# Kernel tuning notes

Hardware: AMD Instinct MI355X
Metric: run time of the kernel (lower is better)

## Reference

```python
import jax, jax.numpy as jnp
import numpy as np

SCENE = (128, 128, 8)      # (X, Y, Z) voxel grid
VOXEL_SIZE = 0.4
DOWNSAMPLE_Z = 2
NUM_HEADS = 8
NUM_POINTS = 4
LN_EPS = 1e-5


def _pix2vox(depth, K, E, voxel_origin):
    # depth [1,H,W]; K [1,3,3]; E [1,4,4]; voxel_origin [1,3]
    B, H, W = depth.shape
    gx, gy = jnp.meshgrid(jnp.arange(W, dtype=depth.dtype), jnp.arange(H, dtype=depth.dtype))
    pix = jnp.stack([gx, gy])                              # [2,H,W] -> (u, v) after flip in torch
    d = depth[:, None]                                     # [B,1,H,W]
    p_x = jnp.concatenate([pix[None] * d, d], 1).reshape(B, 3, -1)
    p_c = jnp.linalg.inv(K) @ p_x                          # camera coords [B,3,HW]
    p_c = jnp.concatenate([p_c, jnp.ones_like(p_c[:, :1])], 1)
    p_w = jnp.linalg.inv(E) @ p_c                          # world coords [B,4,HW]
    p_v = (jnp.swapaxes(p_w[:, :3], 1, 2) - voxel_origin[:, None, :]) / VOXEL_SIZE - 0.5
    p_v = p_v.at[..., 2].set(p_v[..., 2] / DOWNSAMPLE_Z)
    return jnp.trunc(p_v).astype(jnp.int32)               # torch .long() truncates toward 0


def _voxel_mask(p_v):
    X, Y, Z = SCENE
    p = p_v[0]                                             # [HW,3] (batch asserted == 1)
    valid = ((p[:, 0] >= 0) & (p[:, 0] < X) & (p[:, 1] >= 0) & (p[:, 1] < Y)
             & (p[:, 2] >= 0) & (p[:, 2] < Z))
    flat = jnp.where(valid, (p[:, 0] * Y + p[:, 1]) * Z + p[:, 2], 0)
    return jnp.zeros(X * Y * Z, dtype=bool).at[flat].max(valid)


def _ms_deform_attn(q, feats, ref, Wv, bv, Woff, boff, Wattw, battw, Wout, bout):
    # q [N,C]; feats: list of [C,Hl,Wl]; ref [N,2] normalized (shared across levels)
    N, C = q.shape
    hd = C // NUM_HEADS
    shapes = [(f.shape[1], f.shape[2]) for f in feats]
    L = len(feats)
    flat = jnp.concatenate([f.reshape(C, -1).T for f in feats], 0)      # [Lsum, C]
    value = (flat @ Wv.T + bv).reshape(-1, NUM_HEADS, hd)               # [Lsum, h, hd]
    off = (q @ Woff.T + boff).reshape(N, NUM_HEADS, L, NUM_POINTS, 2)
    w = jax.nn.softmax((q @ Wattw.T + battw).reshape(N, NUM_HEADS, L * NUM_POINTS), -1)
    w = w.reshape(N, NUM_HEADS, L, NUM_POINTS)
    normalizer = jnp.array([[wl, hl] for (hl, wl) in shapes], dtype=q.dtype)  # (W,H) per level
    loc = ref[:, None, None, None, :] + off / normalizer[None, None, :, None, :]
    h_idx = jnp.arange(NUM_HEADS)[None, :, None]
    out = jnp.zeros((N, NUM_HEADS, hd), q.dtype)
    start = 0
    for lvl, (Hl, Wl) in enumerate(shapes):
        v = value[start:start + Hl * Wl]                   # [Hl*Wl, h, hd]
        start += Hl * Wl
        # grid_sample bilinear, align_corners=False, zero padding
        x = loc[:, :, lvl, :, 0] * Wl - 0.5                # [N,h,P]
        y = loc[:, :, lvl, :, 1] * Hl - 0.5
        x0 = jnp.floor(x); y0 = jnp.floor(y)
        lx = x - x0; ly = y - y0
        x0i = x0.astype(jnp.int32); y0i = y0.astype(jnp.int32)
        samp = jnp.zeros((N, NUM_HEADS, NUM_POINTS, hd), q.dtype)
        for dy, dx, wgt in ((0, 0, (1 - lx) * (1 - ly)), (0, 1, lx * (1 - ly)),
                            (1, 0, (1 - lx) * ly), (1, 1, lx * ly)):
            xi = x0i + dx; yi = y0i + dy
            ok = (xi >= 0) & (xi < Wl) & (yi >= 0) & (yi < Hl)
            idx = jnp.where(ok, yi * Wl + xi, 0)
            g = v[idx, h_idx]                              # [N,h,P,hd] per-head gather
            samp = samp + g * (wgt * ok)[..., None]
        out = out + jnp.einsum('nhp,nhpd->nhd', w[:, :, lvl], samp)
    return out.reshape(N, C) @ Wout.T + bout


def _forward(scene_embed, feat0, feat1, feat2, depth, K, E, voxel_origin, ref_pix,
             Wv, bv, Woff, boff, Wattw, battw, Wout, bout, ln_g, ln_b):
    X, Y, Z = SCENE
    mask = _voxel_mask(_pix2vox(depth, K, E, voxel_origin))             # [N] bool
    q = scene_embed[0]                                                  # [N,C]
    attn = _ms_deform_attn(q, [feat0[0], feat1[0], feat2[0]], ref_pix[0],
                           Wv, bv, Woff, boff, Wattw, battw, Wout, bout)
    h = q + attn                                                        # residual (MSDeformAttn identity)
    mu = jnp.mean(h, -1, keepdims=True)
    var = jnp.mean((h - mu) ** 2, -1, keepdims=True)
    h = (h - mu) / jnp.sqrt(var + LN_EPS) * ln_g + ln_b                 # post-norm
    out = jnp.where(mask[:, None], h, q)                                # index_fov_back_to_voxels
    return out.T.reshape(1, -1, X, Y, Z)                                # nlc -> nchw [1,C,X,Y,Z]


def setup_inputs() -> dict:
    key = jax.random.key(0)
    ks = jax.random.split(key, 12)
    X, Y, Z = SCENE
    N = X * Y * Z
    C = 128
    H, W = 192, 640
    s = 0.02
    scene_embed = jax.random.normal(ks[0], (1, N, C), jnp.float32)
    feat0 = jax.random.normal(ks[1], (1, C, 48, 160), jnp.float32)
    feat1 = jax.random.normal(ks[2], (1, C, 24, 80), jnp.float32)
    feat2 = jax.random.normal(ks[3], (1, C, 12, 40), jnp.float32)
    depth = jax.random.uniform(ks[4], (1, H, W), jnp.float32, 1.0, 40.0)
    K = jnp.array([[[552.55, 0.0, 320.0], [0.0, 552.55, 96.0], [0.0, 0.0, 1.0]]], jnp.float32)
    E = jnp.eye(4, dtype=jnp.float32)[None]
    voxel_origin = jnp.array([[-25.6, -3.2, 0.0]], jnp.float32)
    ref_pix = jax.random.uniform(ks[5], (1, N, 2), jnp.float32)
    return {
        'scene_embed': scene_embed, 'feat0': feat0, 'feat1': feat1, 'feat2': feat2,
        'depth': depth, 'K': K, 'E': E, 'voxel_origin': voxel_origin, 'ref_pix': ref_pix,
        'Wv': jax.random.normal(ks[6], (C, C), jnp.float32) * s,
        'bv': jnp.zeros((C,), jnp.float32),
        'Woff': jax.random.normal(ks[7], (NUM_HEADS * 3 * NUM_POINTS * 2, C), jnp.float32) * s,
        'boff': jnp.zeros((NUM_HEADS * 3 * NUM_POINTS * 2,), jnp.float32),
        'Wattw': jax.random.normal(ks[8], (NUM_HEADS * 3 * NUM_POINTS, C), jnp.float32) * s,
        'battw': jnp.zeros((NUM_HEADS * 3 * NUM_POINTS,), jnp.float32),
        'Wout': jax.random.normal(ks[9], (C, C), jnp.float32) * s,
        'bout': jnp.zeros((C,), jnp.float32),
        'ln_g': jnp.ones((C,), jnp.float32),
        'ln_b': jnp.zeros((C,), jnp.float32),
    }


def reference(scene_embed, feat0, feat1, feat2, depth, K, E, voxel_origin, ref_pix,
              Wv, bv, Woff, boff, Wattw, battw, Wout, bout, ln_g, ln_b):
    return _forward(scene_embed, feat0, feat1, feat2, depth, K, E, voxel_origin, ref_pix,
                    Wv, bv, Woff, boff, Wattw, battw, Wout, bout, ln_g, ln_b)
```

## Files before the change

kernel.cpp:

```cpp
#include <hip/hip_runtime.h>
#include <hip/hip_bf16.h>
#include <stdint.h>

#define XS 128
#define YS 128
#define ZS 8
#define NQ (XS*YS*ZS)
#define CDIM 128
#define NH 8
#define HD 16
#define DH 192
#define DW 640
#define NPIX (DH*DW)
#define NVPIX 10080

typedef float f32x4 __attribute__((ext_vector_type(4)));
typedef short s16x8 __attribute__((ext_vector_type(8)));

__device__ __forceinline__ float b2f(unsigned short u){
    union { unsigned int i; float f; } v; v.i = ((unsigned int)u) << 16; return v.f;
}
__device__ __forceinline__ unsigned short f2b(float f){
    __hip_bfloat16 h = __float2bfloat16(f);
    return *reinterpret_cast<unsigned short*>(&h);
}
__device__ __forceinline__ float blo(unsigned int u){
    union { unsigned int i; float f; } v; v.i = u << 16; return v.f;
}
__device__ __forceinline__ float bhi(unsigned int u){
    union { unsigned int i; float f; } v; v.i = u & 0xffff0000u; return v.f;
}

__global__ __launch_bounds__(256)
void inv_kernel(const float* __restrict__ K,
                const float* __restrict__ E,
                double* __restrict__ inv_out,
                const float* __restrict__ Woff,
                const float* __restrict__ Wattw,
                const float* __restrict__ Wout,
                unsigned short* __restrict__ Wbf){
    if (blockIdx.x != 0){
        int idx = (blockIdx.x-1)*256 + threadIdx.x;
        if (idx < 24576)      Wbf[idx] = f2b(Woff[idx]);
        else if (idx < 36864) Wbf[idx] = f2b(Wattw[idx-24576]);
        else if (idx < 40960) Wbf[idx] = 0;
        else if (idx < 57344) Wbf[idx] = f2b(Wout[idx-40960]);
        return;
    }
    if (threadIdx.x != 0) return;
    double k[3][3], e[4][4];
    for (int i=0;i<9;i++)  k[i/3][i%3] = (double)K[i];
    for (int i=0;i<16;i++) e[i/4][i%4] = (double)E[i];
    double det = k[0][0]*(k[1][1]*k[2][2]-k[1][2]*k[2][1])
               - k[0][1]*(k[1][0]*k[2][2]-k[1][2]*k[2][0])
               + k[0][2]*(k[1][0]*k[2][1]-k[1][1]*k[2][0]);
    double id = 1.0/det;
    double inv[3][3];
    inv[0][0]=(k[1][1]*k[2][2]-k[1][2]*k[2][1])*id;
    inv[0][1]=(k[0][2]*k[2][1]-k[0][1]*k[2][2])*id;
    inv[0][2]=(k[0][1]*k[1][2]-k[0][2]*k[1][1])*id;
    inv[1][0]=(k[1][2]*k[2][0]-k[1][0]*k[2][2])*id;
    inv[1][1]=(k[0][0]*k[2][2]-k[0][2]*k[2][0])*id;
    inv[1][2]=(k[0][2]*k[1][0]-k[0][0]*k[1][2])*id;
    inv[2][0]=(k[1][0]*k[2][1]-k[1][1]*k[2][0])*id;
    inv[2][1]=(k[0][1]*k[2][0]-k[0][0]*k[2][1])*id;
    inv[2][2]=(k[0][0]*k[1][1]-k[0][1]*k[1][0])*id;
    for (int i=0;i<9;i++) inv_out[i] = inv[i/3][i%3];
    double a[4][8];
    for (int i=0;i<4;i++){ for(int j=0;j<4;j++){ a[i][j]=e[i][j]; a[i][4+j]=(i==j)?1.0:0.0; } }
    for (int c=0;c<4;c++){
        int piv=c; double best=fabs(a[c][c]);
        for (int r=c+1;r<4;r++){ double v=fabs(a[r][c]); if (v>best){best=v;piv=r;} }
        if (piv!=c){ for (int j=0;j<8;j++){ double tmp=a[c][j]; a[c][j]=a[piv][j]; a[piv][j]=tmp; } }
        double pv = 1.0/a[c][c];
        for (int j=0;j<8;j++) a[c][j]*=pv;
        for (int r=0;r<4;r++){
            if (r==c) continue;
            double f=a[r][c];
            for(int j=0;j<8;j++) a[r][j]-=f*a[c][j];
        }
    }
    for (int i=0;i<16;i++) inv_out[9+i] = a[i/4][4 + (i%4)];
}

__global__ __launch_bounds__(256)
void prep2_kernel(int nVal,
                  const float* __restrict__ f0,
                  const float* __restrict__ f1,
                  const float* __restrict__ f2,
                  const float* __restrict__ Wv,
                  const float* __restrict__ bv,
                  unsigned short* __restrict__ value,
                  const float* __restrict__ depth,
                  const double* __restrict__ invm,
                  const float* __restrict__ vorigin,
                  unsigned char* __restrict__ mask){
    __shared__ float fl2[2][CDIM][4];
    const int t = threadIdx.x;
    if ((int)blockIdx.x < nVal){
        const int half = t >> 7, tt = t & 127;
        const int p0 = blockIdx.x*8 + half*4;
        float (*fl)[4] = fl2[half];
        const float* src; int hw, lp;
        if (p0 < 7680)      { src=f0; hw=7680; lp=p0; }
        else if (p0 < 9600) { src=f1; hw=1920; lp=p0-7680; }
        else                { src=f2; hw=480;  lp=p0-9600; }
        float4 v = *(const float4*)(src + tt*hw + lp);
        fl[tt][0]=v.x; fl[tt][1]=v.y; fl[tt][2]=v.z; fl[tt][3]=v.w;
        __syncthreads();
        float bb = bv[tt];
        float acc[4] = {bb,bb,bb,bb};
        const float4* wrow = (const float4*)(Wv + tt*CDIM);
        #pragma unroll 8
        for (int kc=0; kc<32; ++kc){
            float4 w = wrow[kc];
            #pragma unroll
            for (int u=0;u<4;u++){
                float wu = (u==0)?w.x:(u==1)?w.y:(u==2)?w.z:w.w;
                float4 fv = *(const float4*)fl[kc*4+u];
                acc[0] += fv.x*wu; acc[1] += fv.y*wu; acc[2] += fv.z*wu; acc[3] += fv.w*wu;
            }
        }
        const int hh = tt >> 4, cc = tt & 15;
        #pragma unroll
        for (int i=0;i<4;i++)
            value[((size_t)hh*NVPIX + (size_t)(p0+i))*HD + cc] = f2b(acc[i]);
    } else {
        int tid = (blockIdx.x - nVal)*256 + t;
        if (tid >= NPIX) return;
        int gx = tid % DW, gy = tid / DW;
        double d  = (double)depth[tid];
        double X0 = (double)gx * d, X1 = (double)gy * d, X2 = d;
        double c0 = invm[0]*X0 + invm[1]*X1 + invm[2]*X2;
        double c1 = invm[3]*X0 + invm[4]*X1 + invm[5]*X2;
        double c2 = invm[6]*X0 + invm[7]*X1 + invm[8]*X2;
        const double* iE = invm + 9;
        double w0 = iE[0]*c0 + iE[1]*c1 + iE[2]*c2  + iE[3];
        double w1 = iE[4]*c0 + iE[5]*c1 + iE[6]*c2  + iE[7];
        double w2 = iE[8]*c0 + iE[9]*c1 + iE[10]*c2 + iE[11];
        double v0 = (w0-(double)vorigin[0])/0.4 - 0.5;
        double v1 = (w1-(double)vorigin[1])/0.4 - 0.5;
        double v2 = ((w2-(double)vorigin[2])/0.4 - 0.5) / 2.0;
        int xi = (int)v0, yi = (int)v1, zi = (int)v2;
        if (xi>=0 && xi<XS && yi>=0 && yi<YS && zi>=0 && zi<ZS)
            mask[(xi*YS + yi)*ZS + zi] = 1;
    }
}

__global__ __launch_bounds__(256, 2)
void attn_fused(const float* __restrict__ q_in,
                const float* __restrict__ refpix,
                const unsigned short* __restrict__ Wbf,
                const float* __restrict__ boff,
                const float* __restrict__ battw,
                const unsigned short* __restrict__ value,
                const unsigned short* __restrict__ WoutBf,
                const float* __restrict__ bout,
                const float* __restrict__ lng,
                const float* __restrict__ lnb,
                const unsigned char* __restrict__ mask,
                float* __restrict__ dout){
    const int nq0 = blockIdx.x * 32;
    const int t = threadIdx.x;
    __shared__ __align__(16) unsigned char smem[36384];
    unsigned short* Ob    = (unsigned short*)smem;
    unsigned char*  qbfB  = smem + 18432;
    unsigned char*  descB = smem + 18432;
    float*          out2  = (float*)(smem + 18432);
    unsigned char*  obfB  = smem + 30720;
    float*          bias  = (float*)(smem + 34816);
    float*          rp_s  = (float*)(smem + 35968);
    unsigned char*  mask_s= smem + 36224;
    float*          wredp = (float*)(smem + 36256);

    #pragma unroll
    for (int i=0;i<4;i++){
        int idx = t + i*256;
        int row = idx >> 5, c4 = idx & 31;
        float4 qv = ((const float4*)(q_in + (size_t)(nq0+row)*CDIM))[c4];
        unsigned int pk0 = (unsigned int)f2b(qv.x) | ((unsigned int)f2b(qv.y)<<16);
        unsigned int pk1 = (unsigned int)f2b(qv.z) | ((unsigned int)f2b(qv.w)<<16);
        unsigned int bo = ((unsigned int)(row*256 + c4*8)) ^ (unsigned int)((row&7)<<4);
        *(unsigned int*)(qbfB + bo)     = pk0;
        *(unsigned int*)(qbfB + bo + 4) = pk1;
    }
    for (int i=t;i<288;i+=256) bias[i] = (i<192)? boff[i] : battw[i-192];
    ((unsigned int*)obfB)[512 + t] = 0;
    ((unsigned int*)obfB)[768 + t] = 0;
    if (t < 64) rp_s[t] = refpix[nq0*2 + t];
    if (t < 32) mask_s[t] = mask[nq0 + t];
    __syncthreads();

    {
        const int w = t >> 6, lane = t & 63, lr = lane & 15, lg = lane >> 4;
        const int nt0 = w*5;
        f32x4 acc[5][2];
        #pragma unroll
        for (int j=0;j<5;j++){ acc[j][0]=(f32x4){0,0,0,0}; acc[j][1]=(f32x4){0,0,0,0}; }
        #pragma unroll
        for (int ks=0; ks<4; ++ks){
            s16x8 bf[2];
            #pragma unroll
            for (int qt=0;qt<2;qt++){
                int qrow = qt*16 + lr;
                unsigned int bo = ((unsigned int)(qrow*256 + ks*64 + lg*16)) ^ (unsigned int)((qrow&7)<<4);
                bf[qt] = *(const s16x8*)(qbfB + bo);
            }
            const unsigned short* wp = Wbf + (size_t)(nt0*16 + lr)*CDIM + ks*32 + lg*8;
            #pragma unroll
            for (int j=0;j<5;++j){
                s16x8 af = *(const s16x8*)(wp + j*16*CDIM);
                acc[j][0] = __builtin_amdgcn_mfma_f32_16x16x32_bf16(af, bf[0], acc[j][0], 0, 0, 0);
                acc[j][1] = __builtin_amdgcn_mfma_f32_16x16x32_bf16(af, bf[1], acc[j][1], 0, 0, 0);
            }
        }
        #pragma unroll
        for (int j=0;j<5;++j){
            int nt = nt0 + j;
            if (nt < 18){
                #pragma unroll
                for (int qt=0;qt<2;qt++){
                    int q = qt*16 + lr;
                    int base = (q>>3)*2304 + (q&7);
                    #pragma unroll
                    for (int r=0;r<4;++r){
                        int f = nt*16 + lg*4 + r;
                        Ob[base + f*8] = f2b(acc[j][qt][r] + bias[f]);
                    }
                }
            }
        }
    }
    __syncthreads();

    {
        int q = t >> 3, h = t & 7;
        unsigned short* p = Ob + (q>>3)*2304 + (192 + h*12)*8 + (q&7);
        float e[12]; float m = -1e30f;
        #pragma unroll
        for (int i=0;i<12;i++){ e[i] = b2f(p[i*8]); m = fmaxf(m, e[i]); }
        float s = 0.f;
        #pragma unroll
        for (int i=0;i<12;i++){ e[i] = __expf(e[i]-m); s += e[i]; }
        float is = 1.f/s;
        #pragma unroll
        for (int i=0;i<12;i++) p[i*8] = f2b(e[i]*is);
    }
    __syncthreads();

    for (int sr = 0; sr < 4; ++sr){
        const unsigned short* raw = Ob + sr*2304;
        const int nsr = nq0 + sr*8;

        for (int idx = t; idx < 768; idx += 256){
            int q = idx & 7, hp = idx >> 3;
            int lp = hp % 12;
            float fw, fh; int Wl, Hl, st;
            if (lp < 4)      { fw=160.f; fh=48.f; Wl=160; Hl=48; st=0; }
            else if (lp < 8) { fw=80.f;  fh=24.f; Wl=80;  Hl=24; st=7680; }
            else             { fw=40.f;  fh=12.f; Wl=40;  Hl=12; st=9600; }
            float offx = b2f(raw[(hp*2)*8 + q]);
            float offy = b2f(raw[(hp*2+1)*8 + q]);
            float aw   = b2f(raw[(192+hp)*8 + q]);
            float x = rp_s[(sr*8+q)*2+0]*fw - 0.5f + offx;
            float y = rp_s[(sr*8+q)*2+1]*fh - 0.5f + offy;
            float x0f = floorf(x), y0f = floorf(y);
            float lx = x-x0f, ly = y-y0f;
            int x0 = (int)x0f, y0 = (int)y0f;
            bool x0ok = (x0>=0)&&(x0<Wl), x1ok=(x0+1>=0)&&(x0+1<Wl);
            bool y0ok = (y0>=0)&&(y0<Hl), y1ok=(y0+1>=0)&&(y0+1<Hl);
            float w00 = (x0ok&&y0ok)? (1.f-lx)*(1.f-ly)*aw : 0.f;
            float w01 = (x1ok&&y0ok)? lx*(1.f-ly)*aw       : 0.f;
            float w10 = (x0ok&&y1ok)? (1.f-lx)*ly*aw       : 0.f;
            float w11 = (x1ok&&y1ok)? lx*ly*aw             : 0.f;
            int yc0 = min(max(y0,0),Hl-1), yc1 = min(max(y0+1,0),Hl-1);
            int xc0 = min(max(x0,0),Wl-1), xc1 = min(max(x0+1,0),Wl-1);
            unsigned int rb0 = (unsigned int)(st + yc0*Wl), rb1 = (unsigned int)(st + yc1*Wl);
            uint4 d;
            d.x = (rb0+(unsigned int)xc0) | ((rb0+(unsigned int)xc1)<<16);
            d.y = (rb1+(unsigned int)xc0) | ((rb1+(unsigned int)xc1)<<16);
            d.z = (unsigned int)f2b(w00) | ((unsigned int)f2b(w01)<<16);
            d.w = (unsigned int)f2b(w10) | ((unsigned int)f2b(w11)<<16);
            *(uint4*)(descB + (((unsigned int)(idx ^ ((idx>>5)&7)))<<4)) = d;
        }
        __syncthreads();

        {
            const int cp = t & 7, hs = (t>>3) & 7, qgs = t >> 6;
            const unsigned int vbase = (unsigned int)hs*(NVPIX*HD*2) + (unsigned int)cp*4;
            const char* vb = (const char*)value;
            float av0x=0.f, av0y=0.f, av1x=0.f, av1y=0.f;
            #pragma unroll
            for (int lp=0; lp<12; ++lp){
                #pragma unroll
                for (int qi2=0; qi2<2; ++qi2){
                    int idx = (hs*12+lp)*8 + qgs*2 + qi2;
                    uint4 d = *(const uint4*)(descB + (((unsigned int)(idx ^ ((idx>>5)&7)))<<4));
                    unsigned int o00 = vbase + ((d.x & 0xffffu)<<5);
                    unsigned int o01 = vbase + ((d.x >> 16)<<5);
                    unsigned int o10 = vbase + ((d.y & 0xffffu)<<5);
                    unsigned int o11 = vbase + ((d.y >> 16)<<5);
                    unsigned int u00 = *(const unsigned int*)(vb + o00);
                    unsigned int u01 = *(const unsigned int*)(vb + o01);
                    unsigned int u10 = *(const unsigned int*)(vb + o10);
                    unsigned int u11 = *(const unsigned int*)(vb + o11);
                    float w00 = blo(d.z), w01 = bhi(d.z), w10 = blo(d.w), w11 = bhi(d.w);
                    float sx = blo(u00)*w00 + blo(u01)*w01 + blo(u10)*w10 + blo(u11)*w11;
                    float sy = bhi(u00)*w00 + bhi(u01)*w01 + bhi(u10)*w10 + bhi(u11)*w11;
                    if (qi2 == 0){ av0x += sx; av0y += sy; }
                    else         { av1x += sx; av1y += sy; }
                }
            }
            const int q0q = qgs*2;
            unsigned int pk0 = (unsigned int)f2b(av0x) | ((unsigned int)f2b(av0y)<<16);
            unsigned int pk1 = (unsigned int)f2b(av1x) | ((unsigned int)f2b(av1y)<<16);
            unsigned int bo0 = (unsigned int)(q0q*256 + hs*32 + cp*4)     ^ (unsigned int)((q0q&7)<<4);
            unsigned int bo1 = (unsigned int)((q0q+1)*256 + hs*32 + cp*4) ^ (unsigned int)(((q0q+1)&7)<<4);
            *(unsigned int*)(obfB + bo0) = pk0;
            *(unsigned int*)(obfB + bo1) = pk1;
        }
        __syncthreads();

        {
            const int w = t >> 6, lane = t & 63, lr = lane & 15, lg = lane >> 4;
            f32x4 a0 = (f32x4){0.f,0.f,0.f,0.f};
            f32x4 a1 = (f32x4){0.f,0.f,0.f,0.f};
            #pragma unroll
            for (int ks=0; ks<4; ++ks){
                unsigned int bo = (unsigned int)(lr*256 + ks*64 + lg*16) ^ (unsigned int)((lr&7)<<4);
                s16x8 bfrag = *(const s16x8*)(obfB + bo);
                const unsigned short* wp = WoutBf + (size_t)(w*32 + lr)*CDIM + ks*32 + lg*8;
                s16x8 af0 = *(const s16x8*)(wp);
                s16x8 af1 = *(const s16x8*)(wp + 16*CDIM);
                a0 = __builtin_amdgcn_mfma_f32_16x16x32_bf16(af0, bfrag, a0, 0, 0, 0);
                a1 = __builtin_amdgcn_mfma_f32_16x16x32_bf16(af1, bfrag, a1, 0, 0, 0);
            }
            if (lr < 8){
                int f0 = w*32 + lg*4;
                float4 b0 = *(const float4*)(bout + f0);
                float4 b1 = *(const float4*)(bout + f0 + 16);
                float4 v0, v1;
                v0.x = a0[0]+b0.x; v0.y = a0[1]+b0.y; v0.z = a0[2]+b0.z; v0.w = a0[3]+b0.w;
                v1.x = a1[0]+b1.x; v1.y = a1[1]+b1.y; v1.z = a1[2]+b1.z; v1.w = a1[3]+b1.w;
                *(float4*)(out2 + lr*CDIM + f0)      = v0;
                *(float4*)(out2 + lr*CDIM + f0 + 16) = v1;
            }
        }
        __syncthreads();

        {
            const int r = t & 127;
            const int qb = t >> 7;
            const int wv = t >> 6;
            float qv[4], hv[4], s1[4], s2[4];
            #pragma unroll
            for (int qi4=0;qi4<4;qi4++){
                qv[qi4] = q_in[(size_t)(nsr + qb*4 + qi4)*CDIM + r];
                hv[qi4] = qv[qi4] + out2[(qb*4+qi4)*CDIM + r];
                s1[qi4] = hv[qi4];
                s2[qi4] = hv[qi4]*hv[qi4];
            }
            #pragma unroll
            for (int off=32; off>0; off>>=1){
                #pragma unroll
                for (int qi4=0;qi4<4;qi4++){
                    s1[qi4] += __shfl_xor(s1[qi4], off, 64);
                    s2[qi4] += __shfl_xor(s2[qi4], off, 64);
                }
            }
            if ((t&63)==0){
                #pragma unroll
                for (int qi4=0;qi4<4;qi4++){
                    wredp[0*16 + wv*4 + qi4] = s1[qi4];
                    wredp[1*16 + wv*4 + qi4] = s2[qi4];
                }
            }
            __syncthreads();

            float res[4];
            const float g = lng[r], b = lnb[r];
            #pragma unroll
            for (int qi4=0;qi4<4;qi4++){
                float mu  = (wredp[0*16 + (qb*2)*4 + qi4] + wredp[0*16 + (qb*2+1)*4 + qi4]) * (1.f/128.f);
                float msq = (wredp[1*16 + (qb*2)*4 + qi4] + wredp[1*16 + (qb*2+1)*4 + qi4]) * (1.f/128.f);
                float var = msq - mu*mu;
                float nv  = (hv[qi4]-mu) * __frsqrt_rn(var + 1e-5f) * g + b;
                res[qi4] = mask_s[sr*8 + qb*4+qi4] ? nv : qv[qi4];
            }
            float4 o; o.x=res[0]; o.y=res[1]; o.z=res[2]; o.w=res[3];
            *(float4*)(dout + (size_t)r*NQ + nsr + qb*4) = o;
        }
        __syncthreads();
    }
}

extern "C" void kernel_launch(void* const* d_in, const int* in_sizes, int n_in,
                              void* d_out, int out_size, void* d_ws, size_t ws_size,
                              hipStream_t stream){
    const float* scene  = (const float*)d_in[0];
    const float* f0     = (const float*)d_in[1];
    const float* f1     = (const float*)d_in[2];
    const float* f2     = (const float*)d_in[3];
    const float* depth  = (const float*)d_in[4];
    const float* K      = (const float*)d_in[5];
    const float* E      = (const float*)d_in[6];
    const float* vorig  = (const float*)d_in[7];
    const float* refpix = (const float*)d_in[8];
    const float* Wv     = (const float*)d_in[9];
    const float* bv     = (const float*)d_in[10];
    const float* Woff   = (const float*)d_in[11];
    const float* boff   = (const float*)d_in[12];
    const float* Wattw  = (const float*)d_in[13];
    const float* battw  = (const float*)d_in[14];
    const float* Wout   = (const float*)d_in[15];
    const float* bout   = (const float*)d_in[16];
    const float* lng    = (const float*)d_in[17];
    const float* lnb    = (const float*)d_in[18];

    char* ws = (char*)d_ws;
    double*         invm   = (double*)(ws);
    unsigned char*  mask   = (unsigned char*)(ws + 512);
    unsigned short* value  = (unsigned short*)(ws + 512 + 131072);
    unsigned short* Wbf    = (unsigned short*)(ws + 512 + 131072 + 2580480);
    unsigned short* WoutBf = Wbf + 40960;

    hipMemsetAsync(mask, 0, NQ, stream);
    inv_kernel<<<225, 256, 0, stream>>>(K, E, invm, Woff, Wattw, Wout, Wbf);

    int nVal  = NVPIX/8;
    int nMask = (NPIX+255)/256;
    prep2_kernel<<<nVal + nMask, 256, 0, stream>>>(nVal, f0, f1, f2, Wv, bv, value,
                                                   depth, invm, vorig, mask);
    attn_fused<<<NQ/32, 256, 0, stream>>>(scene, refpix, Wbf, boff, battw, value,
                                          WoutBf, bout, lng, lnb, mask,
                                          (float*)d_out);
}
```

Baseline: 401.8 us.

## Merge prep kernels and widen bilinear gather to 16-byte value loads

Folds the matrix-inverse and weight-conversion kernel into the value/mask prep kernel. Each mask block now recomputes the K and E inverses in shared memory, which removes one launch and the dependency between the two. In the attention gather, each thread now loads 16-byte chunks (8 channels) for one row pair of a sampling point instead of 4-byte loads for four corners, then combines the two row halves with a lane shuffle. The query load is hoisted ahead of the gather so its latency overlaps it. In exchange, each mask block repeats a serial double-precision inverse, and the gather has more register pressure.

```diff
diff --git a/kernel.cpp b/kernel.cpp
--- a/kernel.cpp
+++ b/kernel.cpp
@@ -16,6 +16,7 @@
 
 typedef float f32x4 __attribute__((ext_vector_type(4)));
 typedef short s16x8 __attribute__((ext_vector_type(8)));
+typedef unsigned int u32x4 __attribute__((ext_vector_type(4)));
 
 __device__ __forceinline__ float b2f(unsigned short u){
     union { unsigned int i; float f; } v; v.i = ((unsigned int)u) << 16; return v.f;
@@ -32,75 +33,35 @@
 }
 
 __global__ __launch_bounds__(256)
-void inv_kernel(const float* __restrict__ K,
-                const float* __restrict__ E,
-                double* __restrict__ inv_out,
-                const float* __restrict__ Woff,
-                const float* __restrict__ Wattw,
-                const float* __restrict__ Wout,
-                unsigned short* __restrict__ Wbf){
-    if (blockIdx.x != 0){
-        int idx = (blockIdx.x-1)*256 + threadIdx.x;
+void prep_kernel(int nW, int nVal,
+                 const float* __restrict__ Woff,
+                 const float* __restrict__ Wattw,
+                 const float* __restrict__ Wout,
+                 unsigned short* __restrict__ Wbf,
+                 const float* __restrict__ f0,
+                 const float* __restrict__ f1,
+                 const float* __restrict__ f2,
+                 const float* __restrict__ Wv,
+                 const float* __restrict__ bv,
+                 unsigned short* __restrict__ value,
+                 const float* __restrict__ depth,
+                 const float* __restrict__ K,
+                 const float* __restrict__ E,
+                 const float* __restrict__ vorigin,
+                 unsigned char* __restrict__ mask){
+    __shared__ __align__(16) unsigned char smem[16384];
+    const int t = threadIdx.x;
+
+    if ((int)blockIdx.x < nW){
+        int idx = blockIdx.x*256 + t;
         if (idx < 24576)      Wbf[idx] = f2b(Woff[idx]);
         else if (idx < 36864) Wbf[idx] = f2b(Wattw[idx-24576]);
         else if (idx < 40960) Wbf[idx] = 0;
         else if (idx < 57344) Wbf[idx] = f2b(Wout[idx-40960]);
-        return;
-    }
-    if (threadIdx.x != 0) return;
-    double k[3][3], e[4][4];
-    for (int i=0;i<9;i++)  k[i/3][i%3] = (double)K[i];
-    for (int i=0;i<16;i++) e[i/4][i%4] = (double)E[i];
-    double det = k[0][0]*(k[1][1]*k[2][2]-k[1][2]*k[2][1])
-               - k[0][1]*(k[1][0]*k[2][2]-k[1][2]*k[2][0])
-               + k[0][2]*(k[1][0]*k[2][1]-k[1][1]*k[2][0]);
-    double id = 1.0/det;
-    double inv[3][3];
-    inv[0][0]=(k[1][1]*k[2][2]-k[1][2]*k[2][1])*id;
-    inv[0][1]=(k[0][2]*k[2][1]-k[0][1]*k[2][2])*id;
-    inv[0][2]=(k[0][1]*k[1][2]-k[0][2]*k[1][1])*id;
-    inv[1][0]=(k[1][2]*k[2][0]-k[1][0]*k[2][2])*id;
-    inv[1][1]=(k[0][0]*k[2][2]-k[0][2]*k[2][0])*id;
-    inv[1][2]=(k[0][2]*k[1][0]-k[0][0]*k[1][2])*id;
-    inv[2][0]=(k[1][0]*k[2][1]-k[1][1]*k[2][0])*id;
-    inv[2][1]=(k[0][1]*k[2][0]-k[0][0]*k[2][1])*id;
-    inv[2][2]=(k[0][0]*k[1][1]-k[0][1]*k[1][0])*id;
-    for (int i=0;i<9;i++) inv_out[i] = inv[i/3][i%3];
-    double a[4][8];
-    for (int i=0;i<4;i++){ for(int j=0;j<4;j++){ a[i][j]=e[i][j]; a[i][4+j]=(i==j)?1.0:0.0; } }
-    for (int c=0;c<4;c++){
-        int piv=c; double best=fabs(a[c][c]);
-        for (int r=c+1;r<4;r++){ double v=fabs(a[r][c]); if (v>best){best=v;piv=r;} }
-        if (piv!=c){ for (int j=0;j<8;j++){ double tmp=a[c][j]; a[c][j]=a[piv][j]; a[piv][j]=tmp; } }
-        double pv = 1.0/a[c][c];
-        for (int j=0;j<8;j++) a[c][j]*=pv;
-        for (int r=0;r<4;r++){
-            if (r==c) continue;
-            double f=a[r][c];
-            for(int j=0;j<8;j++) a[r][j]-=f*a[c][j];
-        }
-    }
-    for (int i=0;i<16;i++) inv_out[9+i] = a[i/4][4 + (i%4)];
-}
-
-__global__ __launch_bounds__(256)
-void prep2_kernel(int nVal,
-                  const float* __restrict__ f0,
-                  const float* __restrict__ f1,
-                  const float* __restrict__ f2,
-                  const float* __restrict__ Wv,
-                  const float* __restrict__ bv,
-                  unsigned short* __restrict__ value,
-                  const float* __restrict__ depth,
-                  const double* __restrict__ invm,
-                  const float* __restrict__ vorigin,
-                  unsigned char* __restrict__ mask){
-    __shared__ float fl2[2][CDIM][4];
-    const int t = threadIdx.x;
-    if ((int)blockIdx.x < nVal){
+    } else if ((int)blockIdx.x < nW + nVal){
         const int half = t >> 7, tt = t & 127;
-        const int p0 = blockIdx.x*8 + half*4;
-        float (*fl)[4] = fl2[half];
+        const int p0 = (blockIdx.x - nW)*8 + half*4;
+        float (*fl)[4] = (float(*)[4])(smem + half*2048);
         const float* src; int hw, lp;
         if (p0 < 7680)      { src=f0; hw=7680; lp=p0; }
         else if (p0 < 9600) { src=f1; hw=1920; lp=p0-7680; }
@@ -126,15 +87,50 @@
         for (int i=0;i<4;i++)
             value[((size_t)hh*NVPIX + (size_t)(p0+i))*HD + cc] = f2b(acc[i]);
     } else {
-        int tid = (blockIdx.x - nVal)*256 + t;
+        double* invs = (double*)smem;
+        if (t == 0){
+            double k[3][3], e[4][4];
+            for (int i=0;i<9;i++)  k[i/3][i%3] = (double)K[i];
+            for (int i=0;i<16;i++) e[i/4][i%4] = (double)E[i];
+            double det = k[0][0]*(k[1][1]*k[2][2]-k[1][2]*k[2][1])
+                       - k[0][1]*(k[1][0]*k[2][2]-k[1][2]*k[2][0])
+                       + k[0][2]*(k[1][0]*k[2][1]-k[1][1]*k[2][0]);
+            double id = 1.0/det;
+            invs[0]=(k[1][1]*k[2][2]-k[1][2]*k[2][1])*id;
+            invs[1]=(k[0][2]*k[2][1]-k[0][1]*k[2][2])*id;
+            invs[2]=(k[0][1]*k[1][2]-k[0][2]*k[1][1])*id;
+            invs[3]=(k[1][2]*k[2][0]-k[1][0]*k[2][2])*id;
+            invs[4]=(k[0][0]*k[2][2]-k[0][2]*k[2][0])*id;
+            invs[5]=(k[0][2]*k[1][0]-k[0][0]*k[1][2])*id;
+            invs[6]=(k[1][0]*k[2][1]-k[1][1]*k[2][0])*id;
+            invs[7]=(k[0][1]*k[2][0]-k[0][0]*k[2][1])*id;
+            invs[8]=(k[0][0]*k[1][1]-k[0][1]*k[1][0])*id;
+            double a[4][8];
+            for (int i=0;i<4;i++){ for(int j=0;j<4;j++){ a[i][j]=e[i][j]; a[i][4+j]=(i==j)?1.0:0.0; } }
+            for (int c=0;c<4;c++){
+                int piv=c; double best=fabs(a[c][c]);
+                for (int r=c+1;r<4;r++){ double v=fabs(a[r][c]); if (v>best){best=v;piv=r;} }
+                if (piv!=c){ for (int j=0;j<8;j++){ double tmp=a[c][j]; a[c][j]=a[piv][j]; a[piv][j]=tmp; } }
+                double pv = 1.0/a[c][c];
+                for (int j=0;j<8;j++) a[c][j]*=pv;
+                for (int r=0;r<4;r++){
+                    if (r==c) continue;
+                    double f=a[r][c];
+                    for(int j=0;j<8;j++) a[r][j]-=f*a[c][j];
+                }
+            }
+            for (int i=0;i<12;i++) invs[9+i] = a[i/4][4 + (i%4)];
+        }
+        __syncthreads();
+        int tid = ((int)blockIdx.x - nW - nVal)*256 + t;
         if (tid >= NPIX) return;
         int gx = tid % DW, gy = tid / DW;
         double d  = (double)depth[tid];
         double X0 = (double)gx * d, X1 = (double)gy * d, X2 = d;
-        double c0 = invm[0]*X0 + invm[1]*X1 + invm[2]*X2;
-        double c1 = invm[3]*X0 + invm[4]*X1 + invm[5]*X2;
-        double c2 = invm[6]*X0 + invm[7]*X1 + invm[8]*X2;
-        const double* iE = invm + 9;
+        double c0 = invs[0]*X0 + invs[1]*X1 + invs[2]*X2;
+        double c1 = invs[3]*X0 + invs[4]*X1 + invs[5]*X2;
+        double c2 = invs[6]*X0 + invs[7]*X1 + invs[8]*X2;
+        const double* iE = invs + 9;
         double w0 = iE[0]*c0 + iE[1]*c1 + iE[2]*c2  + iE[3];
         double w1 = iE[4]*c0 + iE[5]*c1 + iE[6]*c2  + iE[7];
         double w2 = iE[8]*c0 + iE[9]*c1 + iE[10]*c2 + iE[11];
@@ -285,39 +281,50 @@
         }
         __syncthreads();
 
+        float qv[4];
         {
-            const int cp = t & 7, hs = (t>>3) & 7, qgs = t >> 6;
-            const unsigned int vbase = (unsigned int)hs*(NVPIX*HD*2) + (unsigned int)cp*4;
+            const int r = t & 127, qb = t >> 7;
+            #pragma unroll
+            for (int qi4=0;qi4<4;qi4++)
+                qv[qi4] = q_in[(size_t)(nsr + qb*4 + qi4)*CDIM + r];
+        }
+
+        {
+            const int cs  = t & 1;
+            const int cp2 = (t >> 1) & 1;
+            const int hs  = (t >> 2) & 7;
+            const int qq  = t >> 5;
+            const unsigned int vbase = (unsigned int)hs*(NVPIX*HD*2) + (unsigned int)cp2*16;
             const char* vb = (const char*)value;
-            float av0x=0.f, av0y=0.f, av1x=0.f, av1y=0.f;
+            float a8[8] = {0.f,0.f,0.f,0.f,0.f,0.f,0.f,0.f};
             #pragma unroll
             for (int lp=0; lp<12; ++lp){
+                int idx = (hs*12+lp)*8 + qq;
+                uint4 d = *(const uint4*)(descB + (((unsigned int)(idx ^ ((idx>>5)&7)))<<4));
+                unsigned int pidx = cs ? d.y : d.x;
+                unsigned int wpk  = cs ? d.w : d.z;
+                unsigned int oa = vbase + ((pidx & 0xffffu)<<5);
+                unsigned int ob = vbase + ((pidx >> 16)<<5);
+                u32x4 ua = *(const u32x4*)(vb + oa);
+                u32x4 ub = *(const u32x4*)(vb + ob);
+                float wa = blo(wpk), wb = bhi(wpk);
                 #pragma unroll
-                for (int qi2=0; qi2<2; ++qi2){
-                    int idx = (hs*12+lp)*8 + qgs*2 + qi2;
-                    uint4 d = *(const uint4*)(descB + (((unsigned int)(idx ^ ((idx>>5)&7)))<<4));
-                    unsigned int o00 = vbase + ((d.x & 0xffffu)<<5);
-                    unsigned int o01 = vbase + ((d.x >> 16)<<5);
-                    unsigned int o10 = vbase + ((d.y & 0xffffu)<<5);
-                    unsigned int o11 = vbase + ((d.y >> 16)<<5);
-                    unsigned int u00 = *(const unsigned int*)(vb + o00);
-                    unsigned int u01 = *(const unsigned int*)(vb + o01);
-                    unsigned int u10 = *(const unsigned int*)(vb + o10);
-                    unsigned int u11 = *(const unsigned int*)(vb + o11);
-                    float w00 = blo(d.z), w01 = bhi(d.z), w10 = blo(d.w), w11 = bhi(d.w);
-                    float sx = blo(u00)*w00 + blo(u01)*w01 + blo(u10)*w10 + blo(u11)*w11;
-                    float sy = bhi(u00)*w00 + bhi(u01)*w01 + bhi(u10)*w10 + bhi(u11)*w11;
-                    if (qi2 == 0){ av0x += sx; av0y += sy; }
-                    else         { av1x += sx; av1y += sy; }
+                for (int j=0;j<4;j++){
+                    a8[2*j]   += blo(ua[j])*wa + blo(ub[j])*wb;
+                    a8[2*j+1] += bhi(ua[j])*wa + bhi(ub[j])*wb;
                 }
             }
-            const int q0q = qgs*2;
-            unsigned int pk0 = (unsigned int)f2b(av0x) | ((unsigned int)f2b(av0y)<<16);
-            unsigned int pk1 = (unsigned int)f2b(av1x) | ((unsigned int)f2b(av1y)<<16);
-            unsigned int bo0 = (unsigned int)(q0q*256 + hs*32 + cp*4)     ^ (unsigned int)((q0q&7)<<4);
-            unsigned int bo1 = (unsigned int)((q0q+1)*256 + hs*32 + cp*4) ^ (unsigned int)(((q0q+1)&7)<<4);
-            *(unsigned int*)(obfB + bo0) = pk0;
-            *(unsigned int*)(obfB + bo1) = pk1;
+            #pragma unroll
+            for (int j=0;j<8;j++) a8[j] += __shfl_xor(a8[j], 1, 64);
+            if (cs == 0){
+                u32x4 pk;
+                pk[0] = (unsigned int)f2b(a8[0]) | ((unsigned int)f2b(a8[1])<<16);
+                pk[1] = (unsigned int)f2b(a8[2]) | ((unsigned int)f2b(a8[3])<<16);
+                pk[2] = (unsigned int)f2b(a8[4]) | ((unsigned int)f2b(a8[5])<<16);
+                pk[3] = (unsigned int)f2b(a8[6]) | ((unsigned int)f2b(a8[7])<<16);
+                unsigned int bo = ((unsigned int)(qq*256 + hs*32 + cp2*16)) ^ (unsigned int)((qq&7)<<4);
+                *(u32x4*)(obfB + bo) = pk;
+            }
         }
         __syncthreads();
 
@@ -352,10 +359,9 @@
             const int r = t & 127;
             const int qb = t >> 7;
             const int wv = t >> 6;
-            float qv[4], hv[4], s1[4], s2[4];
+            float hv[4], s1[4], s2[4];
             #pragma unroll
             for (int qi4=0;qi4<4;qi4++){
-                qv[qi4] = q_in[(size_t)(nsr + qb*4 + qi4)*CDIM + r];
                 hv[qi4] = qv[qi4] + out2[(qb*4+qi4)*CDIM + r];
                 s1[qi4] = hv[qi4];
                 s2[qi4] = hv[qi4]*hv[qi4];
@@ -418,19 +424,20 @@
     const float* lnb    = (const float*)d_in[18];
 
     char* ws = (char*)d_ws;
-    double*         invm   = (double*)(ws);
     unsigned char*  mask   = (unsigned char*)(ws + 512);
     unsigned short* value  = (unsigned short*)(ws + 512 + 131072);
     unsigned short* Wbf    = (unsigned short*)(ws + 512 + 131072 + 2580480);
     unsigned short* WoutBf = Wbf + 40960;
 
     hipMemsetAsync(mask, 0, NQ, stream);
-    inv_kernel<<<225, 256, 0, stream>>>(K, E, invm, Woff, Wattw, Wout, Wbf);
-
+
+    int nW    = 57344/256;
     int nVal  = NVPIX/8;
     int nMask = (NPIX+255)/256;
-    prep2_kernel<<<nVal + nMask, 256, 0, stream>>>(nVal, f0, f1, f2, Wv, bv, value,
-                                                   depth, invm, vorig, mask);
+    prep_kernel<<<nW + nVal + nMask, 256, 0, stream>>>(
+        nW, nVal, Woff, Wattw, Wout, Wbf,
+        f0, f1, f2, Wv, bv, value,
+        depth, K, E, vorig, mask);
     attn_fused<<<NQ/32, 256, 0, stream>>>(scene, refpix, Wbf, boff, battw, value,
                                           WoutBf, bout, lng, lnb, mask,
                                           (float*)d_out);
```

Result: no change. 402.1 us (+0.1%).
